# Performance work log

Measured on AMD Instinct MI355X. Metric: run time of the kernel, lower is better.

The kernel has to match this reference:

```python
import jax, jax.numpy as jnp
import numpy as np

B, L, G, K, HID, CLS = 256, 1000, 300, 19, 100, 2  # batch, seq len, num_cnns, kernel, per-unit hidden, classes
P = L // 10  # pooled length = per-group input features = 100
EPS = 1e-5


def setup_inputs() -> dict:
    key = jax.random.key(0)
    ks = jax.random.split(key, 24)
    u = lambda k, s: jax.random.uniform(k, s, jnp.float32, 0.5, 1.5)
    n = lambda k, s, sc=0.1: jax.random.normal(k, s, jnp.float32) * sc
    return {
        "x": jax.random.normal(ks[0], (B, 4, L), jnp.float32),
        # motif scanner conv: [out=G, in=4, k=19]
        "conv_w": n(ks[1], (G, 4, K)),
        "conv_b": n(ks[2], (G,)),
        "bn1_g": u(ks[3], (G,)), "bn1_b": n(ks[4], (G,)),
        "bn1_m": n(ks[5], (G,)), "bn1_v": u(ks[6], (G,)),
        # grouped 1x1 conv #1: per-group [HID <- P]
        "W1": n(ks[7], (G, HID, P)),
        "b1": n(ks[8], (G, HID)),
        "bn2_g": u(ks[9], (G, HID)), "bn2_b": n(ks[10], (G, HID)),
        "bn2_m": n(ks[11], (G, HID)), "bn2_v": u(ks[12], (G, HID)),
        # grouped 1x1 conv #2: per-group [1 <- HID]
        "W2": n(ks[13], (G, HID)),
        "b2": n(ks[14], (G,)),
        "bn3_g": u(ks[15], (G,)), "bn3_b": n(ks[16], (G,)),
        "bn3_m": n(ks[17], (G,)), "bn3_v": u(ks[18], (G,)),
        # final classifier Linear(G, CLS)
        "cls_w": n(ks[19], (CLS, G)),
        "cls_b": n(ks[20], (CLS,)),
    }


def reference(x, conv_w, conv_b, bn1_g, bn1_b, bn1_m, bn1_v,
              W1, b1, bn2_g, bn2_b, bn2_m, bn2_v,
              W2, b2, bn3_g, bn3_b, bn3_m, bn3_v,
              cls_w, cls_b):
    # Conv1d(4->G, k=19, pad=9): same-length output [B, G, L]
    h = jax.lax.conv_general_dilated(
        x, conv_w, window_strides=(1,), padding=[(K // 2, K // 2)],
        dimension_numbers=("NCH", "OIH", "NCH")) + conv_b[None, :, None]
    # BatchNorm1d (inference) + ReLU
    s1 = bn1_g / jnp.sqrt(bn1_v + EPS)
    h = jax.nn.relu((h - bn1_m[None, :, None]) * s1[None, :, None] + bn1_b[None, :, None])
    # MaxPool1d(10): L divisible by 10 -> reshape-max  [B, G, P]
    h = h.reshape(B, G, P, 10).max(-1)
    # Flatten+Unsqueeze+grouped 1x1 conv == block-diagonal matmul per group
    h1 = jnp.einsum("bgi,ghi->bgh", h, W1) + b1            # [B, G, HID]
    h1 = jax.nn.relu((h1 - bn2_m) * (bn2_g / jnp.sqrt(bn2_v + EPS)) + bn2_b)
    # Dropout(0.3) is identity at inference
    h2 = jnp.einsum("bgh,gh->bg", h1, W2) + b2             # [B, G]
    h2 = jax.nn.relu((h2 - bn3_m) * (bn3_g / jnp.sqrt(bn3_v + EPS)) + bn3_b)
    # classifier
    return h2 @ cls_w.T + cls_b                            # [B, CLS]
```

## Files before the change

kernel.cpp:

```cpp
#include <hip/hip_runtime.h>


typedef unsigned short ushort_t;
typedef short short8 __attribute__((ext_vector_type(8)));
typedef float floatx4 __attribute__((ext_vector_type(4)));

constexpr float EPSf = 1e-5f;

__device__ __forceinline__ ushort_t f2bf(float f) {
    unsigned u = __float_as_uint(f);
    unsigned r = (u + 0x7FFFu + ((u >> 16) & 1u)) >> 16;
    return (ushort_t)r;
}

__global__ __launch_bounds__(256) void prep_x(const float* __restrict__ x, ushort_t* __restrict__ xph) {
    int idx = blockIdx.x * 256 + threadIdx.x;
    if (idx >= 256 * 16 * 1040) return;
    int i = idx % 1040, r = idx / 1040;
    int c = r & 3, phi = (r >> 2) & 3, b = r >> 4;
    int src = i + phi - 9;
    float v = ((unsigned)src < 1000u) ? x[b * 4000 + c * 1000 + src] : 0.f;
    xph[idx] = f2bf(v);
}

__global__ __launch_bounds__(256) void prep_wc(const float* __restrict__ conv_w, ushort_t* __restrict__ Wc) {
    int idx = blockIdx.x * 256 + threadIdx.x;
    if (idx >= 2 * 12 * 160 * 8) return;
    int j = idx & 7, gl = (idx >> 3) % 160, kc = ((idx >> 3) / 160) % 12, z = idx / (12 * 160 * 8);
    int g = z * 160 + gl, k = kc * 8 + j, c = k / 24, t = k - c * 24;
    float v = (g < 300 && t < 19) ? conv_w[g * 76 + c * 19 + t] : 0.f;
    Wc[idx] = f2bf(v);
}

__global__ __launch_bounds__(256) void prep_consts(
    const float* __restrict__ b1, const float* __restrict__ g2, const float* __restrict__ be2,
    const float* __restrict__ m2, const float* __restrict__ v2, const float* __restrict__ W2,
    const float* __restrict__ conv_b, const float* __restrict__ g1, const float* __restrict__ be1,
    const float* __restrict__ m1, const float* __restrict__ v1,
    const float* __restrict__ b2, const float* __restrict__ g3, const float* __restrict__ be3,
    const float* __restrict__ m3, const float* __restrict__ v3,
    float* __restrict__ A2, float* __restrict__ C2, float* __restrict__ w2s,
    float* __restrict__ A1, float* __restrict__ B1, float* __restrict__ A3, float* __restrict__ C3) {
    int idx = blockIdx.x * 256 + threadIdx.x;
    if (idx >= 300 * 112) return;
    int h = idx % 112, g = idx / 112;
    float a2 = 0.f, c2 = 0.f, w2v = 0.f;
    if (h < 100) {
        int q = g * 100 + h;
        a2 = g2[q] * rsqrtf(v2[q] + EPSf);
        c2 = (b1[q] - m2[q]) * a2 + be2[q];
        w2v = W2[q];
    }
    A2[idx] = a2; C2[idx] = c2; w2s[idx] = w2v;
    if (h == 0) {
        float a1 = g1[g] * rsqrtf(v1[g] + EPSf);
        A1[g] = a1; B1[g] = (conv_b[g] - m1[g]) * a1 + be1[g];
        float a3 = g3[g] * rsqrtf(v3[g] + EPSf);
        A3[g] = a3; C3[g] = (b2[g] - m3[g]) * a3 + be3[g];
    }
}

__global__ __launch_bounds__(256, 2) void conv_mfma(
    const ushort_t* __restrict__ xph, const ushort_t* __restrict__ Wc,
    const float* __restrict__ A1, const float* __restrict__ B1,
    ushort_t* __restrict__ pooled) {
    __shared__ ushort_t Wl[12 * 160 * 8];
    __shared__ ushort_t xl[16 * 1040];
    __shared__ float A1s[160], B1s[160];

    const int tid = threadIdx.x;
    const int b = blockIdx.x, yw = blockIdx.y, z = blockIdx.z;
    const int gz0 = z * 160;

    {
        const uint4* wsrc = (const uint4*)(Wc + z * 12 * 160 * 8);
        uint4* wdst = (uint4*)Wl;
        for (int i = tid; i < 12 * 160; i += 256) wdst[i] = wsrc[i];
        const uint4* xsrc = (const uint4*)(xph + b * 16 * 1040);
        uint4* xdst = (uint4*)xl;
        for (int i = tid; i < 16 * 1040 / 8; i += 256) xdst[i] = xsrc[i];
        for (int i = tid; i < 160; i += 256) {
            int g = gz0 + i;
            A1s[i] = (g < 300) ? A1[g] : 0.f;
            B1s[i] = (g < 300) ? B1[g] : 0.f;
        }
    }
    __syncthreads();

    const int w = tid >> 6, lane = tid & 63;
    const int p0 = yw * 64 + w * 16;
    if (p0 >= 100) return;
    const int row = lane & 15, quad = lane >> 4;
    const int p_r = p0 + row;
    const int prc = (p_r < 100) ? p_r : 99;

    uint4 af[10][3];
#pragma unroll
    for (int s = 0; s < 3; ++s) {
        int k0 = s * 32 + quad * 8;
        int c = k0 / 24, t0 = k0 - c * 24;
        int base0 = 10 * prc + t0;
        const ushort_t* xc = &xl[c * 1040];
#pragma unroll
        for (int d = 0; d < 10; ++d) {
            int base = base0 + d;
            int phi = base & 3, bi = base - phi;
            const ushort_t* p = xc + phi * 4160 + bi;
            uint2 lo = *(const uint2*)p;
            uint2 hi = *(const uint2*)(p + 4);
            af[d][s] = (uint4){lo.x, lo.y, hi.x, hi.y};
        }
    }

    const int NT = z ? 9 : 10;
    for (int gt = 0; gt < NT; ++gt) {
        short8 bf[3];
#pragma unroll
        for (int s = 0; s < 3; ++s) {
            uint4 t = *(const uint4*)&Wl[(((s * 4 + quad) * 160) + gt * 16 + row) * 8];
            bf[s] = __builtin_bit_cast(short8, t);
        }
        const float a1v = A1s[gt * 16 + row], b1v = B1s[gt * 16 + row];
        floatx4 mx = {0.f, 0.f, 0.f, 0.f};
#pragma unroll
        for (int d = 0; d < 10; ++d) {
            floatx4 acc = {0.f, 0.f, 0.f, 0.f};
#pragma unroll
            for (int s = 0; s < 3; ++s)
                acc = __builtin_amdgcn_mfma_f32_16x16x32_bf16(
                    __builtin_bit_cast(short8, af[d][s]), bf[s], acc, 0, 0, 0);
#pragma unroll
            for (int r = 0; r < 4; ++r)
                mx[r] = fmaxf(mx[r], fmaf(acc[r], a1v, b1v));
        }
        const int g = gz0 + gt * 16 + row;
        const int pr0 = p0 + quad * 4;
        if (g < 300 && pr0 < 100) {
            ushort4 o = make_ushort4(f2bf(mx[0]), f2bf(mx[1]), f2bf(mx[2]), f2bf(mx[3]));
            *(ushort4*)&pooled[((size_t)b * 300 + g) * 100 + pr0] = o;
        }
    }
}

__global__ __launch_bounds__(256, 2) void mlp_mfma(
    const ushort_t* __restrict__ pooled, const float* __restrict__ W1,
    const float* __restrict__ A2c, const float* __restrict__ C2c, const float* __restrict__ w2c,
    const float* __restrict__ A3, const float* __restrict__ C3,
    float* __restrict__ h2ws) {
    __shared__ ushort_t W1l[16 * 112 * 8];
    __shared__ ushort_t pl[128 * 128];
    __shared__ float A2s[112], C2s[112], w2sl[112];
    __shared__ float sA3, sC3;

    const int tid = threadIdx.x;
    const int g = blockIdx.x, b0 = blockIdx.y * 128;

    {
        uint4* wd = (uint4*)W1l;
        for (int i = tid; i < 16 * 112; i += 256) wd[i] = (uint4){0, 0, 0, 0};
    }
    __syncthreads();
    for (int q = tid; q < 2500; q += 256) {
        int base = q * 4;
        int h = base / 100, i = base - h * 100;
        float4 v = *(const float4*)&W1[(size_t)g * 10000 + base];
        ushort4 o = make_ushort4(f2bf(v.x), f2bf(v.y), f2bf(v.z), f2bf(v.w));
        *(ushort4*)&W1l[((i >> 3) * 112 + h) * 8 + (i & 7)] = o;
    }
    for (int q = tid; q < 128 * 16; q += 256) {
        int bl = q >> 4, kc = q & 15;
        const ushort_t* src = pooled + ((size_t)(b0 + bl) * 300 + g) * 100 + kc * 8;
        uint2 lo = *(const uint2*)src;
        uint2 hi = *(const uint2*)(src + 4);
        int swz = kc ^ (bl & 7);
        *(uint4*)&pl[((bl * 16) + swz) * 8] = (uint4){lo.x, lo.y, hi.x, hi.y};
    }
    if (tid < 112) {
        A2s[tid] = A2c[g * 112 + tid];
        C2s[tid] = C2c[g * 112 + tid];
        w2sl[tid] = w2c[g * 112 + tid];
    }
    if (tid == 0) { sA3 = A3[g]; sC3 = C3[g]; }
    __syncthreads();

    const int w = tid >> 6, lane = tid & 63;
    const int col = lane & 15, quad = lane >> 4;

    short8 bfr[7][4];
#pragma unroll
    for (int nt = 0; nt < 7; ++nt)
#pragma unroll
        for (int s = 0; s < 4; ++s) {
            uint4 t = *(const uint4*)&W1l[(((s * 4 + quad) * 112) + nt * 16 + col) * 8];
            bfr[nt][s] = __builtin_bit_cast(short8, t);
        }

#pragma unroll
    for (int mi = 0; mi < 2; ++mi) {
        const int mt = w * 2 + mi;
        const int bl = mt * 16 + col;
        uint4 afr[4];
#pragma unroll
        for (int s = 0; s < 4; ++s) {
            int kc = s * 4 + quad;
            afr[s] = *(const uint4*)&pl[((bl * 16) + (kc ^ (bl & 7))) * 8];
        }
        float run0 = 0.f, run1 = 0.f, run2 = 0.f, run3 = 0.f;
#pragma unroll
        for (int nt = 0; nt < 7; ++nt) {
            floatx4 acc = {0.f, 0.f, 0.f, 0.f};
#pragma unroll
            for (int s = 0; s < 4; ++s)
                acc = __builtin_amdgcn_mfma_f32_16x16x32_bf16(
                    __builtin_bit_cast(short8, afr[s]), bfr[nt][s], acc, 0, 0, 0);
            const float a2v = A2s[nt * 16 + col], c2v = C2s[nt * 16 + col], w2v = w2sl[nt * 16 + col];
            run0 += fmaxf(fmaf(acc[0], a2v, c2v), 0.f) * w2v;
            run1 += fmaxf(fmaf(acc[1], a2v, c2v), 0.f) * w2v;
            run2 += fmaxf(fmaf(acc[2], a2v, c2v), 0.f) * w2v;
            run3 += fmaxf(fmaf(acc[3], a2v, c2v), 0.f) * w2v;
        }
#pragma unroll
        for (int m = 1; m <= 8; m <<= 1) {
            run0 += __shfl_xor(run0, m, 64);
            run1 += __shfl_xor(run1, m, 64);
            run2 += __shfl_xor(run2, m, 64);
            run3 += __shfl_xor(run3, m, 64);
        }
        if (col == 0) {
            float4 o;
            o.x = fmaxf(fmaf(run0, sA3, sC3), 0.f);
            o.y = fmaxf(fmaf(run1, sA3, sC3), 0.f);
            o.z = fmaxf(fmaf(run2, sA3, sC3), 0.f);
            o.w = fmaxf(fmaf(run3, sA3, sC3), 0.f);
            *(float4*)&h2ws[g * 256 + b0 + mt * 16 + quad * 4] = o;
        }
    }
}

__global__ __launch_bounds__(64) void classifier_kernel(
    const float* __restrict__ h2ws, const float* __restrict__ cls_w,
    const float* __restrict__ cls_b, float* __restrict__ out) {
    const int b = blockIdx.x, t = threadIdx.x;
    float a0 = 0.f, a1 = 0.f;
    for (int gg = t; gg < 300; gg += 64) {
        float v = h2ws[gg * 256 + b];
        a0 = fmaf(v, cls_w[gg], a0);
        a1 = fmaf(v, cls_w[300 + gg], a1);
    }
#pragma unroll
    for (int off = 32; off; off >>= 1) {
        a0 += __shfl_down(a0, off);
        a1 += __shfl_down(a1, off);
    }
    if (t == 0) {
        out[b * 2 + 0] = a0 + cls_b[0];
        out[b * 2 + 1] = a1 + cls_b[1];
    }
}

extern "C" void kernel_launch(void* const* d_in, const int* in_sizes, int n_in,
                              void* d_out, int out_size, void* d_ws, size_t ws_size,
                              hipStream_t stream) {
    const float* x      = (const float*)d_in[0];
    const float* conv_w = (const float*)d_in[1];
    const float* conv_b = (const float*)d_in[2];
    const float* bn1_g  = (const float*)d_in[3];
    const float* bn1_b  = (const float*)d_in[4];
    const float* bn1_m  = (const float*)d_in[5];
    const float* bn1_v  = (const float*)d_in[6];
    const float* W1     = (const float*)d_in[7];
    const float* b1     = (const float*)d_in[8];
    const float* bn2_g  = (const float*)d_in[9];
    const float* bn2_b  = (const float*)d_in[10];
    const float* bn2_m  = (const float*)d_in[11];
    const float* bn2_v  = (const float*)d_in[12];
    const float* W2     = (const float*)d_in[13];
    const float* b2     = (const float*)d_in[14];
    const float* bn3_g  = (const float*)d_in[15];
    const float* bn3_b  = (const float*)d_in[16];
    const float* bn3_m  = (const float*)d_in[17];
    const float* bn3_v  = (const float*)d_in[18];
    const float* cls_w  = (const float*)d_in[19];
    const float* cls_b  = (const float*)d_in[20];

    char* wsb = (char*)d_ws;
    ushort_t* pooled = (ushort_t*)(wsb);
    ushort_t* xph    = (ushort_t*)(wsb + 15360000);
    ushort_t* Wc     = (ushort_t*)(wsb + 23879680);
    float* A2   = (float*)(wsb + 23941120);
    float* C2   = (float*)(wsb + 24075520);
    float* w2s  = (float*)(wsb + 24209920);
    float* A1   = (float*)(wsb + 24344320);
    float* B1   = (float*)(wsb + 24345520);
    float* A3   = (float*)(wsb + 24346720);
    float* C3   = (float*)(wsb + 24347920);
    float* h2ws = (float*)(wsb + 24349120);

    prep_x<<<dim3((256 * 16 * 1040 + 255) / 256), 256, 0, stream>>>(x, xph);
    prep_wc<<<dim3((2 * 12 * 160 * 8 + 255) / 256), 256, 0, stream>>>(conv_w, Wc);
    prep_consts<<<dim3((300 * 112 + 255) / 256), 256, 0, stream>>>(
        b1, bn2_g, bn2_b, bn2_m, bn2_v, W2,
        conv_b, bn1_g, bn1_b, bn1_m, bn1_v,
        b2, bn3_g, bn3_b, bn3_m, bn3_v,
        A2, C2, w2s, A1, B1, A3, C3);

    conv_mfma<<<dim3(256, 2, 2), 256, 0, stream>>>(xph, Wc, A1, B1, pooled);

    mlp_mfma<<<dim3(300, 2), 256, 0, stream>>>(pooled, W1, A2, C2, w2s, A3, C3, h2ws);

    classifier_kernel<<<dim3(256), 64, 0, stream>>>(h2ws, cls_w, cls_b, (float*)d_out);
}
```

Baseline: 154.4 us.

## Merge prep kernels, fold BN constants into consumers, restructure conv grid

Replaces three prep kernels with one combined prep kernel that also pre-converts W1 to a padded bf16 layout. The BN scale/shift constants are now computed inside the conv and MLP kernels. The conv kernel now runs one 448-thread block per batch covering all 304 channels and all positions, instead of a 256x2x2 grid. This removes launches and the redundant x-tile loads per z/y block, and the MLP no longer converts W1 per batch tile. In exchange the conv grid becomes only 256 blocks with larger LDS use, which may reduce occupancy.

Measured after the change: 152.2 us. Within noise of the previous version (-1.4%).

```diff
diff --git a/kernel.cpp b/kernel.cpp
--- a/kernel.cpp
+++ b/kernel.cpp
@@ -13,83 +13,76 @@
     return (ushort_t)r;
 }
 
-__global__ __launch_bounds__(256) void prep_x(const float* __restrict__ x, ushort_t* __restrict__ xph) {
-    int idx = blockIdx.x * 256 + threadIdx.x;
-    if (idx >= 256 * 16 * 1040) return;
-    int i = idx % 1040, r = idx / 1040;
-    int c = r & 3, phi = (r >> 2) & 3, b = r >> 4;
-    int src = i + phi - 9;
-    float v = ((unsigned)src < 1000u) ? x[b * 4000 + c * 1000 + src] : 0.f;
-    xph[idx] = f2bf(v);
-}
-
-__global__ __launch_bounds__(256) void prep_wc(const float* __restrict__ conv_w, ushort_t* __restrict__ Wc) {
-    int idx = blockIdx.x * 256 + threadIdx.x;
-    if (idx >= 2 * 12 * 160 * 8) return;
-    int j = idx & 7, gl = (idx >> 3) % 160, kc = ((idx >> 3) / 160) % 12, z = idx / (12 * 160 * 8);
-    int g = z * 160 + gl, k = kc * 8 + j, c = k / 24, t = k - c * 24;
-    float v = (g < 300 && t < 19) ? conv_w[g * 76 + c * 19 + t] : 0.f;
-    Wc[idx] = f2bf(v);
-}
-
-__global__ __launch_bounds__(256) void prep_consts(
-    const float* __restrict__ b1, const float* __restrict__ g2, const float* __restrict__ be2,
-    const float* __restrict__ m2, const float* __restrict__ v2, const float* __restrict__ W2,
+constexpr int T1_BLKS = 8320;
+constexpr int T2_BLKS = 114;
+constexpr int T3_BLKS = 4200;
+__global__ __launch_bounds__(256) void prep_all(
+    const float* __restrict__ x, const float* __restrict__ conv_w, const float* __restrict__ W1,
+    ushort_t* __restrict__ xph, ushort_t* __restrict__ Wc, ushort_t* __restrict__ W1b)
+{
+    const int blk = blockIdx.x, t = threadIdx.x;
+    if (blk < T1_BLKS) {
+        int u = blk * 256 + t;
+        int iu = u % 520, r = u / 520;
+        int c = r & 3, phi = (r >> 2) & 3, b = r >> 4;
+        int src = iu * 2 + phi - 9;
+        const float* xb = x + b * 4000 + c * 1000;
+        float v0 = ((unsigned)src < 1000u) ? xb[src] : 0.f;
+        float v1 = ((unsigned)(src + 1) < 1000u) ? xb[src + 1] : 0.f;
+        ((unsigned*)xph)[u] = (unsigned)f2bf(v0) | ((unsigned)f2bf(v1) << 16);
+    } else if (blk < T1_BLKS + T2_BLKS) {
+        int idx = (blk - T1_BLKS) * 256 + t;
+        int j = idx & 7, g = (idx >> 3) % 304, kc = idx / (304 * 8);
+        int k = kc * 8 + j, c = k / 24, tt = k - c * 24;
+        float v = (g < 300 && tt < 19) ? conv_w[g * 76 + c * 19 + tt] : 0.f;
+        Wc[idx] = f2bf(v);
+    } else {
+        int v = (blk - T1_BLKS - T2_BLKS) * 256 + t;
+        int jj = v & 1, r = v >> 1;
+        int h = r % 112, r2 = r / 112;
+        int kc = r2 & 15, g = r2 >> 4;
+        int i0 = kc * 8 + jj * 4;
+        ushort4 o = make_ushort4(0, 0, 0, 0);
+        if (h < 100 && i0 <= 96) {
+            float4 w = *(const float4*)&W1[(size_t)g * 10000 + h * 100 + i0];
+            o = make_ushort4(f2bf(w.x), f2bf(w.y), f2bf(w.z), f2bf(w.w));
+        }
+        *(ushort4*)&W1b[((size_t)(g * 16 + kc) * 112 + h) * 8 + jj * 4] = o;
+    }
+}
+
+__global__ __launch_bounds__(448, 2) void conv_mfma(
+    const ushort_t* __restrict__ xph, const ushort_t* __restrict__ Wc,
     const float* __restrict__ conv_b, const float* __restrict__ g1, const float* __restrict__ be1,
     const float* __restrict__ m1, const float* __restrict__ v1,
-    const float* __restrict__ b2, const float* __restrict__ g3, const float* __restrict__ be3,
-    const float* __restrict__ m3, const float* __restrict__ v3,
-    float* __restrict__ A2, float* __restrict__ C2, float* __restrict__ w2s,
-    float* __restrict__ A1, float* __restrict__ B1, float* __restrict__ A3, float* __restrict__ C3) {
-    int idx = blockIdx.x * 256 + threadIdx.x;
-    if (idx >= 300 * 112) return;
-    int h = idx % 112, g = idx / 112;
-    float a2 = 0.f, c2 = 0.f, w2v = 0.f;
-    if (h < 100) {
-        int q = g * 100 + h;
-        a2 = g2[q] * rsqrtf(v2[q] + EPSf);
-        c2 = (b1[q] - m2[q]) * a2 + be2[q];
-        w2v = W2[q];
-    }
-    A2[idx] = a2; C2[idx] = c2; w2s[idx] = w2v;
-    if (h == 0) {
-        float a1 = g1[g] * rsqrtf(v1[g] + EPSf);
-        A1[g] = a1; B1[g] = (conv_b[g] - m1[g]) * a1 + be1[g];
-        float a3 = g3[g] * rsqrtf(v3[g] + EPSf);
-        A3[g] = a3; C3[g] = (b2[g] - m3[g]) * a3 + be3[g];
-    }
-}
-
-__global__ __launch_bounds__(256, 2) void conv_mfma(
-    const ushort_t* __restrict__ xph, const ushort_t* __restrict__ Wc,
-    const float* __restrict__ A1, const float* __restrict__ B1,
-    ushort_t* __restrict__ pooled) {
-    __shared__ ushort_t Wl[12 * 160 * 8];
+    ushort_t* __restrict__ pooled)
+{
+    __shared__ ushort_t Wl[12 * 304 * 8];
     __shared__ ushort_t xl[16 * 1040];
-    __shared__ float A1s[160], B1s[160];
+    __shared__ float A1s[304], B1s[304];
 
     const int tid = threadIdx.x;
-    const int b = blockIdx.x, yw = blockIdx.y, z = blockIdx.z;
-    const int gz0 = z * 160;
+    const int b = blockIdx.x;
 
     {
-        const uint4* wsrc = (const uint4*)(Wc + z * 12 * 160 * 8);
+        const uint4* wsrc = (const uint4*)Wc;
         uint4* wdst = (uint4*)Wl;
-        for (int i = tid; i < 12 * 160; i += 256) wdst[i] = wsrc[i];
-        const uint4* xsrc = (const uint4*)(xph + b * 16 * 1040);
+        for (int i = tid; i < 3648; i += 448) wdst[i] = wsrc[i];
+        const uint4* xsrc = (const uint4*)(xph + (size_t)b * 16640);
         uint4* xdst = (uint4*)xl;
-        for (int i = tid; i < 16 * 1040 / 8; i += 256) xdst[i] = xsrc[i];
-        for (int i = tid; i < 160; i += 256) {
-            int g = gz0 + i;
-            A1s[i] = (g < 300) ? A1[g] : 0.f;
-            B1s[i] = (g < 300) ? B1[g] : 0.f;
+        for (int i = tid; i < 2080; i += 448) xdst[i] = xsrc[i];
+        if (tid < 304) {
+            if (tid < 300) {
+                float A = g1[tid] * rsqrtf(v1[tid] + EPSf);
+                A1s[tid] = A;
+                B1s[tid] = (conv_b[tid] - m1[tid]) * A + be1[tid];
+            } else { A1s[tid] = 0.f; B1s[tid] = 0.f; }
         }
     }
     __syncthreads();
 
     const int w = tid >> 6, lane = tid & 63;
-    const int p0 = yw * 64 + w * 16;
-    if (p0 >= 100) return;
+    const int p0 = w * 16;
     const int row = lane & 15, quad = lane >> 4;
     const int p_r = p0 + row;
     const int prc = (p_r < 100) ? p_r : 99;
@@ -112,13 +105,12 @@
         }
     }
 
-    const int NT = z ? 9 : 10;
-    for (int gt = 0; gt < NT; ++gt) {
+    for (int gt = 0; gt < 19; ++gt) {
         short8 bf[3];
 #pragma unroll
         for (int s = 0; s < 3; ++s) {
-            uint4 t = *(const uint4*)&Wl[(((s * 4 + quad) * 160) + gt * 16 + row) * 8];
-            bf[s] = __builtin_bit_cast(short8, t);
+            uint4 t4 = *(const uint4*)&Wl[(((s * 4 + quad) * 304) + gt * 16 + row) * 8];
+            bf[s] = __builtin_bit_cast(short8, t4);
         }
         const float a1v = A1s[gt * 16 + row], b1v = B1s[gt * 16 + row];
         floatx4 mx = {0.f, 0.f, 0.f, 0.f};
@@ -133,7 +125,7 @@
             for (int r = 0; r < 4; ++r)
                 mx[r] = fmaxf(mx[r], fmaf(acc[r], a1v, b1v));
         }
-        const int g = gz0 + gt * 16 + row;
+        const int g = gt * 16 + row;
         const int pr0 = p0 + quad * 4;
         if (g < 300 && pr0 < 100) {
             ushort4 o = make_ushort4(f2bf(mx[0]), f2bf(mx[1]), f2bf(mx[2]), f2bf(mx[3]));
@@ -143,29 +135,26 @@
 }
 
 __global__ __launch_bounds__(256, 2) void mlp_mfma(
-    const ushort_t* __restrict__ pooled, const float* __restrict__ W1,
-    const float* __restrict__ A2c, const float* __restrict__ C2c, const float* __restrict__ w2c,
-    const float* __restrict__ A3, const float* __restrict__ C3,
-    float* __restrict__ h2ws) {
+    const ushort_t* __restrict__ pooled, const ushort_t* __restrict__ W1b,
+    const float* __restrict__ b1, const float* __restrict__ g2, const float* __restrict__ be2,
+    const float* __restrict__ m2, const float* __restrict__ v2,
+    const float* __restrict__ W2, const float* __restrict__ b2,
+    const float* __restrict__ g3, const float* __restrict__ be3,
+    const float* __restrict__ m3, const float* __restrict__ v3,
+    float* __restrict__ h2ws)
+{
     __shared__ ushort_t W1l[16 * 112 * 8];
     __shared__ ushort_t pl[128 * 128];
     __shared__ float A2s[112], C2s[112], w2sl[112];
     __shared__ float sA3, sC3;
 
     const int tid = threadIdx.x;
-    const int g = blockIdx.x, b0 = blockIdx.y * 128;
+    const int g = blockIdx.y, b0 = blockIdx.x * 128;
 
     {
-        uint4* wd = (uint4*)W1l;
-        for (int i = tid; i < 16 * 112; i += 256) wd[i] = (uint4){0, 0, 0, 0};
-    }
-    __syncthreads();
-    for (int q = tid; q < 2500; q += 256) {
-        int base = q * 4;
-        int h = base / 100, i = base - h * 100;
-        float4 v = *(const float4*)&W1[(size_t)g * 10000 + base];
-        ushort4 o = make_ushort4(f2bf(v.x), f2bf(v.y), f2bf(v.z), f2bf(v.w));
-        *(ushort4*)&W1l[((i >> 3) * 112 + h) * 8 + (i & 7)] = o;
+        const uint4* src = (const uint4*)(W1b + (size_t)g * 14336);
+        uint4* dst = (uint4*)W1l;
+        for (int i = tid; i < 1792; i += 256) dst[i] = src[i];
     }
     for (int q = tid; q < 128 * 16; q += 256) {
         int bl = q >> 4, kc = q & 15;
@@ -176,11 +165,19 @@
         *(uint4*)&pl[((bl * 16) + swz) * 8] = (uint4){lo.x, lo.y, hi.x, hi.y};
     }
     if (tid < 112) {
-        A2s[tid] = A2c[g * 112 + tid];
-        C2s[tid] = C2c[g * 112 + tid];
-        w2sl[tid] = w2c[g * 112 + tid];
-    }
-    if (tid == 0) { sA3 = A3[g]; sC3 = C3[g]; }
+        float a2 = 0.f, c2 = 0.f, w2v = 0.f;
+        if (tid < 100) {
+            int q = g * 100 + tid;
+            a2 = g2[q] * rsqrtf(v2[q] + EPSf);
+            c2 = (b1[q] - m2[q]) * a2 + be2[q];
+            w2v = W2[q];
+        }
+        A2s[tid] = a2; C2s[tid] = c2; w2sl[tid] = w2v;
+    }
+    if (tid == 0) {
+        float a3 = g3[g] * rsqrtf(v3[g] + EPSf);
+        sA3 = a3; sC3 = (b2[g] - m3[g]) * a3 + be3[g];
+    }
     __syncthreads();
 
     const int w = tid >> 6, lane = tid & 63;
@@ -191,8 +188,8 @@
     for (int nt = 0; nt < 7; ++nt)
 #pragma unroll
         for (int s = 0; s < 4; ++s) {
-            uint4 t = *(const uint4*)&W1l[(((s * 4 + quad) * 112) + nt * 16 + col) * 8];
-            bfr[nt][s] = __builtin_bit_cast(short8, t);
+            uint4 t4 = *(const uint4*)&W1l[(((s * 4 + quad) * 112) + nt * 16 + col) * 8];
+            bfr[nt][s] = __builtin_bit_cast(short8, t4);
         }
 
 #pragma unroll
@@ -287,26 +284,17 @@
     ushort_t* pooled = (ushort_t*)(wsb);
     ushort_t* xph    = (ushort_t*)(wsb + 15360000);
     ushort_t* Wc     = (ushort_t*)(wsb + 23879680);
-    float* A2   = (float*)(wsb + 23941120);
-    float* C2   = (float*)(wsb + 24075520);
-    float* w2s  = (float*)(wsb + 24209920);
-    float* A1   = (float*)(wsb + 24344320);
-    float* B1   = (float*)(wsb + 24345520);
-    float* A3   = (float*)(wsb + 24346720);
-    float* C3   = (float*)(wsb + 24347920);
-    float* h2ws = (float*)(wsb + 24349120);
-
-    prep_x<<<dim3((256 * 16 * 1040 + 255) / 256), 256, 0, stream>>>(x, xph);
-    prep_wc<<<dim3((2 * 12 * 160 * 8 + 255) / 256), 256, 0, stream>>>(conv_w, Wc);
-    prep_consts<<<dim3((300 * 112 + 255) / 256), 256, 0, stream>>>(
-        b1, bn2_g, bn2_b, bn2_m, bn2_v, W2,
-        conv_b, bn1_g, bn1_b, bn1_m, bn1_v,
-        b2, bn3_g, bn3_b, bn3_m, bn3_v,
-        A2, C2, w2s, A1, B1, A3, C3);
-
-    conv_mfma<<<dim3(256, 2, 2), 256, 0, stream>>>(xph, Wc, A1, B1, pooled);
-
-    mlp_mfma<<<dim3(300, 2), 256, 0, stream>>>(pooled, W1, A2, C2, w2s, A3, C3, h2ws);
+    ushort_t* W1b    = (ushort_t*)(wsb + 23938048);
+    float*    h2ws   = (float*)  (wsb + 32539648);
+
+    prep_all<<<dim3(T1_BLKS + T2_BLKS + T3_BLKS), 256, 0, stream>>>(x, conv_w, W1, xph, Wc, W1b);
+
+    conv_mfma<<<dim3(256), 448, 0, stream>>>(
+        xph, Wc, conv_b, bn1_g, bn1_b, bn1_m, bn1_v, pooled);
+
+    mlp_mfma<<<dim3(2, 300), 256, 0, stream>>>(
+        pooled, W1b, b1, bn2_g, bn2_b, bn2_m, bn2_v, W2, b2,
+        bn3_g, bn3_b, bn3_m, bn3_v, h2ws);
 
     classifier_kernel<<<dim3(256), 64, 0, stream>>>(h2ws, cls_w, cls_b, (float*)d_out);
 }
```
